# Kernel optimization log

Hardware: AMD Instinct MI355X
Metric: run time of the kernel (lower is better)

The kernel has to match this reference:

```python
import jax, jax.numpy as jnp
import numpy as np
from jax import lax

T, B, DIN, DLAT = 512, 512, 64, 128


def setup_inputs() -> dict:
    key = jax.random.key(0)
    ks = jax.random.split(key, 8)
    s = 0.1  # keep gate pre-activations in a sane range
    return {
        "seqs": jax.random.normal(ks[0], (T, B, DIN), dtype=jnp.float32),
        "h": jax.random.normal(ks[1], (B, DLAT), dtype=jnp.float32),
        "Wz": jax.random.normal(ks[2], (DLAT, DIN + DLAT), dtype=jnp.float32) * s,
        "bz": jax.random.normal(ks[3], (DLAT,), dtype=jnp.float32) * s,
        "Wr": jax.random.normal(ks[4], (DLAT, DIN + DLAT), dtype=jnp.float32) * s,
        "br": jax.random.normal(ks[5], (DLAT,), dtype=jnp.float32) * s,
        "Wi": jax.random.normal(ks[6], (DLAT, DIN + DLAT), dtype=jnp.float32) * s,
        "bi": jax.random.normal(ks[7], (DLAT,), dtype=jnp.float32) * s,
    }


def reference(seqs, h, Wz, bz, Wr, br, Wi, bi):
    # seqs: [T, B, DIN], h: [B, DLAT]. Returns all hiddens [T+1, B, DLAT].
    def step(h, x):
        merge = jnp.concatenate([h, x], axis=1)          # [B, DLAT+DIN]
        zt = jax.nn.sigmoid(merge @ Wz.T + bz)           # update gate
        rt = jax.nn.sigmoid(merge @ Wr.T + br)           # reset gate
        cand = jnp.tanh(jnp.concatenate([h * rt, x], axis=1) @ Wi.T + bi)
        h_new = (1.0 - zt) * h + zt * cand
        return h_new, h_new

    _, hs = lax.scan(step, h, seqs)                      # hs: [T, B, DLAT]
    return jnp.concatenate([h[None], hs], axis=0)        # [T+1, B, DLAT]
```

## Files before the change

### kernel.cpp

```cpp
#include <hip/hip_runtime.h>
#include <math.h>

#define TT   512
#define BB   512
#define DIN  64
#define DLAT 128
#define KKK  192
#define NBLK 32
#define TCHUNK 16
#define LSTR 140
#define X_ELEMS ((size_t)TT * BB * 384)
#define X_BYTES (X_ELEMS * 2)

typedef _Float16 half8 __attribute__((ext_vector_type(8)));
typedef _Float16 half4 __attribute__((ext_vector_type(4)));
typedef float    f32x4 __attribute__((ext_vector_type(4)));

#define MFMA16(A, B, C) __builtin_amdgcn_mfma_f32_16x16x32_f16((A), (B), (C), 0, 0, 0)

__device__ __forceinline__ float fsigmoid(float x) {
    float e = __builtin_amdgcn_exp2f(-1.44269504f * x);
    return __builtin_amdgcn_rcpf(1.f + e);
}
__device__ __forceinline__ float ftanh(float x) {
    float e = __builtin_amdgcn_exp2f(2.88539008f * x);
    return 1.f - 2.f * __builtin_amdgcn_rcpf(1.f + e);
}
__device__ __forceinline__ half8 cvt8(float4 a, float4 b) {
    return (half8){(_Float16)a.x, (_Float16)a.y, (_Float16)a.z, (_Float16)a.w,
                   (_Float16)b.x, (_Float16)b.y, (_Float16)b.z, (_Float16)b.w};
}
__device__ __forceinline__ half8 ld8(const _Float16* p) {
    half4 lo = *(const half4*)p;
    half4 hi = *(const half4*)(p + 4);
    return __builtin_shufflevector(lo, hi, 0, 1, 2, 3, 4, 5, 6, 7);
}

__global__ __launch_bounds__(256) void xproj(
    const float* __restrict__ seqs,
    const float* __restrict__ Wz, const float* __restrict__ bz,
    const float* __restrict__ Wr, const float* __restrict__ br,
    const float* __restrict__ Wi, const float* __restrict__ bi,
    _Float16* __restrict__ X)
{
    const int tid = threadIdx.x;
    const int w = tid >> 6, l = tid & 63, q = l >> 4, ln = l & 15;
    const int bid = blockIdx.x;
    const int tb  = bid >> 5;
    const int blk = bid & 31;
    const int b0  = blk * 16;

    half8 wzf[2][2], wrf[2][2], wif[2][2];
    float bzv[2], brv[2], biv[2];
    #pragma unroll
    for (int s = 0; s < 2; ++s) {
        const int n = 32 * w + 16 * s + ln;
        #pragma unroll
        for (int kt = 0; kt < 2; ++kt) {
            const int k0 = DLAT + kt * 32 + q * 8;
            wzf[s][kt] = cvt8(*(const float4*)&Wz[n * KKK + k0],
                              *(const float4*)&Wz[n * KKK + k0 + 4]);
            wrf[s][kt] = cvt8(*(const float4*)&Wr[n * KKK + k0],
                              *(const float4*)&Wr[n * KKK + k0 + 4]);
            wif[s][kt] = cvt8(*(const float4*)&Wi[n * KKK + k0],
                              *(const float4*)&Wi[n * KKK + k0 + 4]);
        }
        bzv[s] = bz[n]; brv[s] = br[n]; biv[s] = bi[n];
    }

    for (int tt = 0; tt < TCHUNK; ++tt) {
        const int t = tb * TCHUNK + tt;
        const float* xr = seqs + ((size_t)t * BB + b0 + ln) * DIN + q * 8;
        half8 a0 = cvt8(*(const float4*)xr,        *(const float4*)(xr + 4));
        half8 a1 = cvt8(*(const float4*)(xr + 32), *(const float4*)(xr + 36));

        f32x4 az[2], ar[2], ai[2];
        #pragma unroll
        for (int s = 0; s < 2; ++s) {
            az[s] = (f32x4){bzv[s], bzv[s], bzv[s], bzv[s]};
            ar[s] = (f32x4){brv[s], brv[s], brv[s], brv[s]};
            ai[s] = (f32x4){biv[s], biv[s], biv[s], biv[s]};
        }
        #pragma unroll
        for (int s = 0; s < 2; ++s) {
            az[s] = MFMA16(a0, wzf[s][0], az[s]);
            az[s] = MFMA16(a1, wzf[s][1], az[s]);
            ar[s] = MFMA16(a0, wrf[s][0], ar[s]);
            ar[s] = MFMA16(a1, wrf[s][1], ar[s]);
            ai[s] = MFMA16(a0, wif[s][0], ai[s]);
            ai[s] = MFMA16(a1, wif[s][1], ai[s]);
        }

        half8 o0, o1, o2;
        #pragma unroll
        for (int s = 0; s < 2; ++s)
            #pragma unroll
            for (int i = 0; i < 4; ++i) {
                o0[s * 4 + i] = (_Float16)az[s][i];
                o1[s * 4 + i] = (_Float16)ar[s][i];
                o2[s * 4 + i] = (_Float16)ai[s][i];
            }
        _Float16* xo = X + ((size_t)(t * NBLK + blk) * 256 + tid) * 24;
        *(half8*)xo        = o0;
        *(half8*)(xo +  8) = o1;
        *(half8*)(xo + 16) = o2;
    }
}

__global__ __launch_bounds__(512, 2) void gru_rx(
    const float* __restrict__ h0,
    const float* __restrict__ Wz, const float* __restrict__ Wr,
    const float* __restrict__ Wi,
    const _Float16* __restrict__ X, float* __restrict__ out)
{
    __shared__ __align__(16) _Float16 hA [16][LSTR];
    __shared__ __align__(16) _Float16 hrA[16][LSTR];

    const int tid = threadIdx.x;
    const int w   = tid >> 6;
    const int l   = tid & 63;
    const int q   = l >> 4;
    const int ln  = l & 15;
    const int blk = (int)blockIdx.x;
    const int b0  = blk * 16;
    const int nc  = 16 * w + ln;

    half8 wzf[4], wrf[4], wif[4];
    #pragma unroll
    for (int kt = 0; kt < 4; ++kt) {
        const int k0 = kt * 32 + q * 8;
        wzf[kt] = cvt8(*(const float4*)&Wz[nc * KKK + k0],
                       *(const float4*)&Wz[nc * KKK + k0 + 4]);
        wrf[kt] = cvt8(*(const float4*)&Wr[nc * KKK + k0],
                       *(const float4*)&Wr[nc * KKK + k0 + 4]);
        wif[kt] = cvt8(*(const float4*)&Wi[nc * KKK + k0],
                       *(const float4*)&Wi[nc * KKK + k0 + 4]);
    }

    float h[4];
    #pragma unroll
    for (int i = 0; i < 4; ++i)
        h[i] = h0[(size_t)(b0 + 4 * q + i) * DLAT + nc];

    for (int idx = tid; idx < 16 * DLAT; idx += 512) {
        const int m = idx >> 7, c = idx & 127;
        const float v = h0[(size_t)(b0 + m) * DLAT + c];
        out[(size_t)(b0 + m) * DLAT + c] = v;
        hA[m][c] = (_Float16)v;
    }

    const size_t xslot = (size_t)((w >> 1) * 64 + q * 16 + ln) * 24 + (w & 1) * 4;
    const _Float16* xptr = X + (size_t)blk * 256 * 24 + xslot;
    const size_t xstep = (size_t)NBLK * 256 * 24;

    half4 xc0 = *(const half4*)xptr;
    half4 xc1 = *(const half4*)(xptr + 8);
    half4 xc2 = *(const half4*)(xptr + 16);
    xptr += xstep;

    float* optr = out + (size_t)BB * DLAT + (size_t)(b0 + 4 * q) * DLAT + nc;
    const size_t ostep = (size_t)BB * DLAT;

    __syncthreads();

    for (int t = 0; t < TT; ++t) {
        half4 xn0, xn1, xn2;
        const bool have = (t + 1 < TT);
        if (have) {
            xn0 = *(const half4*)xptr;
            xn1 = *(const half4*)(xptr + 8);
            xn2 = *(const half4*)(xptr + 16);
            xptr += xstep;
        }

        half8 a0 = ld8(&hA[ln][ 0 + q * 8]);
        half8 a1 = ld8(&hA[ln][32 + q * 8]);
        half8 a2 = ld8(&hA[ln][64 + q * 8]);
        half8 a3 = ld8(&hA[ln][96 + q * 8]);

        f32x4 ara = (f32x4){(float)xc1[0], (float)xc1[1], (float)xc1[2], (float)xc1[3]};
        f32x4 arb = (f32x4){0.f, 0.f, 0.f, 0.f};
        f32x4 aza = (f32x4){(float)xc0[0], (float)xc0[1], (float)xc0[2], (float)xc0[3]};
        f32x4 azb = (f32x4){0.f, 0.f, 0.f, 0.f};
        ara = MFMA16(a0, wrf[0], ara);
        arb = MFMA16(a1, wrf[1], arb);
        ara = MFMA16(a2, wrf[2], ara);
        arb = MFMA16(a3, wrf[3], arb);
        aza = MFMA16(a0, wzf[0], aza);
        azb = MFMA16(a1, wzf[1], azb);
        aza = MFMA16(a2, wzf[2], aza);
        azb = MFMA16(a3, wzf[3], azb);
        const f32x4 ar = ara + arb;
        #pragma unroll
        for (int i = 0; i < 4; ++i) {
            const float r = fsigmoid(ar[i]);
            hrA[4 * q + i][nc] = (_Float16)(h[i] * r);
        }

        __syncthreads();

        half8 c0 = ld8(&hrA[ln][ 0 + q * 8]);
        half8 c1 = ld8(&hrA[ln][32 + q * 8]);
        half8 c2 = ld8(&hrA[ln][64 + q * 8]);
        half8 c3 = ld8(&hrA[ln][96 + q * 8]);
        f32x4 aia = (f32x4){(float)xc2[0], (float)xc2[1], (float)xc2[2], (float)xc2[3]};
        f32x4 aib = (f32x4){0.f, 0.f, 0.f, 0.f};
        aia = MFMA16(c0, wif[0], aia);
        aib = MFMA16(c1, wif[1], aib);
        aia = MFMA16(c2, wif[2], aia);
        aib = MFMA16(c3, wif[3], aib);

        const f32x4 az = aza + azb;
        float zz[4];
        #pragma unroll
        for (int i = 0; i < 4; ++i)
            zz[i] = fsigmoid(az[i]);

        const f32x4 ai = aia + aib;
        #pragma unroll
        for (int i = 0; i < 4; ++i) {
            const float cand = ftanh(ai[i]);
            const float hn   = h[i] + zz[i] * (cand - h[i]);
            h[i] = hn;
            hA[4 * q + i][nc] = (_Float16)hn;
            optr[i * DLAT] = hn;
        }
        optr += ostep;

        xc0 = xn0; xc1 = xn1; xc2 = xn2;
        __syncthreads();
    }
}

__global__ __launch_bounds__(256, 1) void gru_mfma(
    const float* __restrict__ seqs, const float* __restrict__ h0,
    const float* __restrict__ bz, const float* __restrict__ br,
    const float* __restrict__ bi,
    const float* __restrict__ Wz, const float* __restrict__ Wr,
    const float* __restrict__ Wi, float* __restrict__ out)
{
    __shared__ __align__(16) _Float16 hA [16][136];
    __shared__ __align__(16) _Float16 hrA[16][136];
    __shared__ __align__(16) _Float16 xb [2][16][72];

    const int tid = threadIdx.x;
    const int w   = tid >> 6;
    const int l   = tid & 63;
    const int q   = l >> 4;
    const int ln  = l & 15;
    const int b0  = (int)blockIdx.x * 16;

    half8 wz[2][6], wr[2][6], wi[2][6];
    #pragma unroll
    for (int s = 0; s < 2; ++s) {
        const int n = 32 * w + 16 * s + ln;
        #pragma unroll
        for (int kt = 0; kt < 6; ++kt) {
            const int k0 = kt * 32 + q * 8;
            wz[s][kt] = cvt8(*(const float4*)&Wz[n * KKK + k0],
                             *(const float4*)&Wz[n * KKK + k0 + 4]);
            wr[s][kt] = cvt8(*(const float4*)&Wr[n * KKK + k0],
                             *(const float4*)&Wr[n * KKK + k0 + 4]);
            wi[s][kt] = cvt8(*(const float4*)&Wi[n * KKK + k0],
                             *(const float4*)&Wi[n * KKK + k0 + 4]);
        }
    }
    float bzv[2], brv[2], biv[2];
    #pragma unroll
    for (int s = 0; s < 2; ++s) {
        const int n = 32 * w + 16 * s + ln;
        bzv[s] = bz[n]; brv[s] = br[n]; biv[s] = bi[n];
    }

    float h[2][4];
    #pragma unroll
    for (int s = 0; s < 2; ++s)
        #pragma unroll
        for (int i = 0; i < 4; ++i)
            h[s][i] = h0[(size_t)(b0 + 4 * q + i) * DLAT + 32 * w + 16 * s + ln];

    for (int idx = tid; idx < 16 * DLAT; idx += 256) {
        const int m = idx >> 7, c = idx & 127;
        const float v = h0[(size_t)(b0 + m) * DLAT + c];
        out[(size_t)(b0 + m) * DLAT + c] = v;
        hA[m][c] = (_Float16)v;
    }
    {
        const int m = tid >> 4, k4 = tid & 15;
        const float4 xv = *(const float4*)&seqs[((size_t)0 * BB + b0 + m) * DIN + k4 * 4];
        *(half4*)&xb[0][m][k4 * 4] =
            (half4){(_Float16)xv.x, (_Float16)xv.y, (_Float16)xv.z, (_Float16)xv.w};
    }
    __syncthreads();

    for (int t = 0; t < TT; ++t) {
        const int p = t & 1;
        float4 xv;
        const int xm = tid >> 4, xk = tid & 15;
        if (t + 1 < TT)
            xv = *(const float4*)&seqs[((size_t)(t + 1) * BB + b0 + xm) * DIN + xk * 4];

        half8 a0 = *(const half8*)&hA[ln][ 0 + q * 8];
        half8 a1 = *(const half8*)&hA[ln][32 + q * 8];
        half8 a2 = *(const half8*)&hA[ln][64 + q * 8];
        half8 a3 = *(const half8*)&hA[ln][96 + q * 8];
        half8 x0 = *(const half8*)&xb[p][ln][ 0 + q * 8];
        half8 x1 = *(const half8*)&xb[p][ln][32 + q * 8];

        f32x4 az[2], ar[2], ai[2];
        #pragma unroll
        for (int s = 0; s < 2; ++s) {
            az[s] = (f32x4){bzv[s], bzv[s], bzv[s], bzv[s]};
            ar[s] = (f32x4){brv[s], brv[s], brv[s], brv[s]};
            ai[s] = (f32x4){biv[s], biv[s], biv[s], biv[s]};
        }
        #pragma unroll
        for (int s = 0; s < 2; ++s) {
            az[s] = MFMA16(x0, wz[s][4], az[s]);
            az[s] = MFMA16(x1, wz[s][5], az[s]);
            ar[s] = MFMA16(x0, wr[s][4], ar[s]);
            ar[s] = MFMA16(x1, wr[s][5], ar[s]);
            ai[s] = MFMA16(x0, wi[s][4], ai[s]);
            ai[s] = MFMA16(x1, wi[s][5], ai[s]);
            az[s] = MFMA16(a0, wz[s][0], az[s]);
            az[s] = MFMA16(a1, wz[s][1], az[s]);
            az[s] = MFMA16(a2, wz[s][2], az[s]);
            az[s] = MFMA16(a3, wz[s][3], az[s]);
            ar[s] = MFMA16(a0, wr[s][0], ar[s]);
            ar[s] = MFMA16(a1, wr[s][1], ar[s]);
            ar[s] = MFMA16(a2, wr[s][2], ar[s]);
            ar[s] = MFMA16(a3, wr[s][3], ar[s]);
        }

        float zz[2][4];
        #pragma unroll
        for (int s = 0; s < 2; ++s)
            #pragma unroll
            for (int i = 0; i < 4; ++i) {
                zz[s][i]      = fsigmoid(az[s][i]);
                const float r = fsigmoid(ar[s][i]);
                hrA[4 * q + i][32 * w + 16 * s + ln] = (_Float16)(h[s][i] * r);
            }

        if (t + 1 < TT)
            *(half4*)&xb[p ^ 1][xm][xk * 4] =
                (half4){(_Float16)xv.x, (_Float16)xv.y, (_Float16)xv.z, (_Float16)xv.w};

        __syncthreads();

        half8 c0 = *(const half8*)&hrA[ln][ 0 + q * 8];
        half8 c1 = *(const half8*)&hrA[ln][32 + q * 8];
        half8 c2 = *(const half8*)&hrA[ln][64 + q * 8];
        half8 c3 = *(const half8*)&hrA[ln][96 + q * 8];
        #pragma unroll
        for (int s = 0; s < 2; ++s) {
            ai[s] = MFMA16(c0, wi[s][0], ai[s]);
            ai[s] = MFMA16(c1, wi[s][1], ai[s]);
            ai[s] = MFMA16(c2, wi[s][2], ai[s]);
            ai[s] = MFMA16(c3, wi[s][3], ai[s]);
        }

        #pragma unroll
        for (int s = 0; s < 2; ++s)
            #pragma unroll
            for (int i = 0; i < 4; ++i) {
                const float cand = ftanh(ai[s][i]);
                const float hn   = h[s][i] + zz[s][i] * (cand - h[s][i]);
                h[s][i] = hn;
                const int m = 4 * q + i, c = 32 * w + 16 * s + ln;
                hA[m][c] = (_Float16)hn;
                out[((size_t)(t + 1) * BB + b0 + m) * DLAT + c] = hn;
            }

        __syncthreads();
    }
}

extern "C" void kernel_launch(void* const* d_in, const int* in_sizes, int n_in,
                              void* d_out, int out_size, void* d_ws, size_t ws_size,
                              hipStream_t stream) {
    const float* seqs = (const float*)d_in[0];
    const float* h0   = (const float*)d_in[1];
    const float* Wz   = (const float*)d_in[2];
    const float* bz   = (const float*)d_in[3];
    const float* Wr   = (const float*)d_in[4];
    const float* br   = (const float*)d_in[5];
    const float* Wi   = (const float*)d_in[6];
    const float* bi   = (const float*)d_in[7];
    float* out = (float*)d_out;

    if (ws_size >= X_BYTES) {
        _Float16* X = (_Float16*)d_ws;
        xproj<<<(TT / TCHUNK) * NBLK, 256, 0, stream>>>(seqs, Wz, bz, Wr, br, Wi, bi, X);
        gru_rx<<<NBLK, 512, 0, stream>>>(h0, Wz, Wr, Wi, X, out);
    } else {
        gru_mfma<<<NBLK, 256, 0, stream>>>(seqs, h0, bz, br, bi, Wz, Wr, Wi, out);
    }
}
```

Measured before the change: 515.2 us.

## Replace rcp with Newton-iterated bit-trick reciprocal, pack fp16 conversions, halve time chunk

```diff
diff --git a/kernel.cpp b/kernel.cpp
--- a/kernel.cpp
+++ b/kernel.cpp
@@ -7,28 +7,47 @@
 #define DLAT 128
 #define KKK  192
 #define NBLK 32
-#define TCHUNK 16
+#define TCHUNK 8
 #define LSTR 140
 #define X_ELEMS ((size_t)TT * BB * 384)
 #define X_BYTES (X_ELEMS * 2)
 
 typedef _Float16 half8 __attribute__((ext_vector_type(8)));
 typedef _Float16 half4 __attribute__((ext_vector_type(4)));
+typedef __fp16   fp16x2 __attribute__((ext_vector_type(2)));
 typedef float    f32x4 __attribute__((ext_vector_type(4)));
 
 #define MFMA16(A, B, C) __builtin_amdgcn_mfma_f32_16x16x32_f16((A), (B), (C), 0, 0, 0)
 
+__device__ __forceinline__ float fastrcp(float t) {
+    float y = __int_as_float(0x7EF311C3 - __float_as_int(t));
+    y = y * (2.f - t * y);
+    y = y * (2.f - t * y);
+    return y;
+}
 __device__ __forceinline__ float fsigmoid(float x) {
     float e = __builtin_amdgcn_exp2f(-1.44269504f * x);
-    return __builtin_amdgcn_rcpf(1.f + e);
+    return fastrcp(1.f + e);
 }
 __device__ __forceinline__ float ftanh(float x) {
     float e = __builtin_amdgcn_exp2f(2.88539008f * x);
-    return 1.f - 2.f * __builtin_amdgcn_rcpf(1.f + e);
+    return 1.f - 2.f * fastrcp(1.f + e);
 }
 __device__ __forceinline__ half8 cvt8(float4 a, float4 b) {
-    return (half8){(_Float16)a.x, (_Float16)a.y, (_Float16)a.z, (_Float16)a.w,
-                   (_Float16)b.x, (_Float16)b.y, (_Float16)b.z, (_Float16)b.w};
+    fp16x2 p0 = __builtin_amdgcn_cvt_pkrtz(a.x, a.y);
+    fp16x2 p1 = __builtin_amdgcn_cvt_pkrtz(a.z, a.w);
+    fp16x2 p2 = __builtin_amdgcn_cvt_pkrtz(b.x, b.y);
+    fp16x2 p3 = __builtin_amdgcn_cvt_pkrtz(b.z, b.w);
+    return (half8){(_Float16)p0[0], (_Float16)p0[1], (_Float16)p1[0], (_Float16)p1[1],
+                   (_Float16)p2[0], (_Float16)p2[1], (_Float16)p3[0], (_Float16)p3[1]};
+}
+__device__ __forceinline__ half8 pk8(const f32x4 a, const f32x4 b) {
+    fp16x2 p0 = __builtin_amdgcn_cvt_pkrtz(a[0], a[1]);
+    fp16x2 p1 = __builtin_amdgcn_cvt_pkrtz(a[2], a[3]);
+    fp16x2 p2 = __builtin_amdgcn_cvt_pkrtz(b[0], b[1]);
+    fp16x2 p3 = __builtin_amdgcn_cvt_pkrtz(b[2], b[3]);
+    return (half8){(_Float16)p0[0], (_Float16)p0[1], (_Float16)p1[0], (_Float16)p1[1],
+                   (_Float16)p2[0], (_Float16)p2[1], (_Float16)p3[0], (_Float16)p3[1]};
 }
 __device__ __forceinline__ half8 ld8(const _Float16* p) {
     half4 lo = *(const half4*)p;
@@ -91,19 +110,10 @@
             ai[s] = MFMA16(a1, wif[s][1], ai[s]);
         }
 
-        half8 o0, o1, o2;
-        #pragma unroll
-        for (int s = 0; s < 2; ++s)
-            #pragma unroll
-            for (int i = 0; i < 4; ++i) {
-                o0[s * 4 + i] = (_Float16)az[s][i];
-                o1[s * 4 + i] = (_Float16)ar[s][i];
-                o2[s * 4 + i] = (_Float16)ai[s][i];
-            }
         _Float16* xo = X + ((size_t)(t * NBLK + blk) * 256 + tid) * 24;
-        *(half8*)xo        = o0;
-        *(half8*)(xo +  8) = o1;
-        *(half8*)(xo + 16) = o2;
+        *(half8*)xo        = pk8(az[0], az[1]);
+        *(half8*)(xo +  8) = pk8(ar[0], ar[1]);
+        *(half8*)(xo + 16) = pk8(ai[0], ai[1]);
     }
 }
 
```

New measurement: 574.7 us. +11.6%, slower.
